# Kernel optimization log

Measured on AMD Instinct MI355X. Metric: run time of the kernel, lower is better.

Reference implementation:

```python
import jax, jax.numpy as jnp
import numpy as np
from jax import lax

NUM_LAYERS = 8
K = 3
C = 128  # residual/gate/skip channels
DIL_H = (1, 2, 4, 8, 1, 2, 4, 8)
DIL_W = (1, 2, 4, 8, 16, 32, 64, 128)
DN = ('NCHW', 'OIHW', 'NCHW')


def _conv(x, w, b, dh=1, dw=1, pad_h=0, pad_w=0):
    # causal along H: pad only on top by pad_h (equivalent to pytorch's
    # symmetric pad + out[:, :, :-pad_h] slice); symmetric along W.
    out = lax.conv_general_dilated(
        x, w, window_strides=(1, 1),
        padding=((pad_h, 0), (pad_w, pad_w)),
        rhs_dilation=(dh, dw), dimension_numbers=DN)
    return out + b[None, :, None, None]


def setup_inputs() -> dict:
    key = jax.random.key(0)
    ks = jax.random.split(key, 6)
    B, H, W = 2, 16, 4096
    return {
        'x': jax.random.normal(ks[0], (B, 1, H, W), jnp.float32),
        'c': jax.random.normal(ks[1], (B, 80, H, W), jnp.float32),
        'front_w': jax.random.normal(ks[2], (C, 1, 1, 1), jnp.float32),
        'front_b': jnp.zeros((C,), jnp.float32),
        'fg_w': jax.random.normal(ks[3], (NUM_LAYERS, 2 * C, C, K, K), jnp.float32) * (1.0 / np.sqrt(C * K * K)),
        'fg_b': jnp.zeros((NUM_LAYERS, 2 * C), jnp.float32),
        'fgc_w': jax.random.normal(ks[4], (NUM_LAYERS, 2 * C, 80, 1, 1), jnp.float32) * (1.0 / np.sqrt(80)),
        'fgc_b': jnp.zeros((NUM_LAYERS, 2 * C), jnp.float32),
        'rs_w': jax.random.normal(ks[5], (NUM_LAYERS, 2 * C, C, 1, 1), jnp.float32) * (1.0 / np.sqrt(C)),
        'rs_b': jnp.zeros((NUM_LAYERS, 2 * C), jnp.float32),
    }


def reference(x, c, front_w, front_b, fg_w, fg_b, fgc_w, fgc_b, rs_w, rs_b):
    # front 1x1 conv (causal but pad_h = 0 for kernel_size=1)
    h = _conv(x, front_w, front_b)  # [B, C, H, W]
    skip = jnp.zeros_like(h)
    for i in range(NUM_LAYERS):
        dh, dw = DIL_H[i], DIL_W[i]
        pad_h = dh * (K - 1)
        pad_w = dw * (K - 1) // 2
        # dilated causal conv -> [B, 2C, H, W]
        hg = _conv(h, fg_w[i], fg_b[i], dh, dw, pad_h, pad_w)
        # 1x1 conditioning conv on c
        cg = _conv(c, fgc_w[i], fgc_b[i])
        a = hg + cg
        acts = jnp.tanh(a[:, :C]) * jax.nn.sigmoid(a[:, C:])
        # 1x1 res/skip conv -> [B, 2C, H, W]
        rs = _conv(acts, rs_w[i], rs_b[i])
        h = h + rs[:, :C]
        skip = skip + rs[:, C:]
    return skip
```

## Files before the change

### kernel.cpp

```cpp
#include <hip/hip_runtime.h>
#include <math.h>

#define NL    8
#define CCH   128
#define CINC  80
#define CPAD  128
#define HH    16
#define WW    4096
#define HW    (HH*WW)
#define PADW  128
#define WWP   (WW + 2*PADW)
#define NT    10
#define PADF  64

#define HBF_N   (2*HH*WWP*CCH)
#define ZROW_N  (WWP*CCH)
#define CT_N    (2*HW*CPAD)
#define SKB_N   (2*HW*CCH)
#define GW_N    (NL*NT*4*16*64*8)
#define RW_N    (NL*4*16*64*8)

using v8s   = __attribute__((ext_vector_type(8))) short;
using f32x4 = __attribute__((ext_vector_type(4))) float;

__device__ __forceinline__ unsigned short f2bf(float f) {
    unsigned int u = __builtin_bit_cast(unsigned int, f);
    u += 0x7fffu + ((u >> 16) & 1u);
    return (unsigned short)(u >> 16);
}
__device__ __forceinline__ float bfu2f(unsigned int v) {
    return __builtin_bit_cast(float, v << 16);
}
__device__ __forceinline__ float gated(float a, float g) {
    float ac = fminf(a, 15.0f);
    float e  = __expf(2.0f * ac);
    float th = (e - 1.0f) * __builtin_amdgcn_rcpf(e + 1.0f);
    float sg = __builtin_amdgcn_rcpf(1.0f + __expf(-g));
    return th * sg;
}

__device__ __forceinline__ void gl_lds16(const void* g, void* l) {
    __builtin_amdgcn_global_load_lds(
        (const __attribute__((address_space(1))) unsigned int*)g,
        (__attribute__((address_space(3))) unsigned int*)l, 16, 0, 0);
}

__device__ __host__ __forceinline__ int tap_of(int t) { return (t < 7) ? t : (t == 8 ? 8 : 7); }

__global__ void prep_weights(const float* __restrict__ fg_w, const float* __restrict__ fgc_w,
                             const float* __restrict__ rs_w,
                             const float* __restrict__ fg_b, const float* __restrict__ fgc_b,
                             const float* __restrict__ rs_b,
                             unsigned short* __restrict__ gw, unsigned short* __restrict__ rw,
                             float* __restrict__ gbias, float* __restrict__ rbias) {
    const int total = GW_N + RW_N + 2 * NL * 256;
    const int stride = gridDim.x * blockDim.x;
    for (int idx = blockIdx.x * blockDim.x + threadIdx.x; idx < total; idx += stride) {
        if (idx < GW_N) {
            int t0 = idx;
            int j = t0 & 7;  t0 >>= 3;
            int l = t0 & 63; t0 >>= 6;
            int mt = t0 & 15; t0 >>= 4;
            int tq = t0 % (NT*4);
            int i  = t0 / (NT*4);
            int t  = tq >> 2, q = tq & 3;
            int m  = mt*16 + (l & 15);
            int oo = (m & 1)*128 + (m >> 1);
            int ci = q*32 + 8*(l >> 4) + j;
            float v;
            if (t == 7) {
                v = (ci < CINC) ? fgc_w[((size_t)i*256 + oo)*CINC + ci] : 0.0f;
            } else {
                int tt = tap_of(t);
                v = fg_w[(((size_t)i*256 + oo)*128 + ci)*9 + tt];
            }
            gw[idx] = f2bf(v);
        } else if (idx < GW_N + RW_N) {
            int t0 = idx - GW_N;
            int j = t0 & 7;  t0 >>= 3;
            int l = t0 & 63; t0 >>= 6;
            int mt = t0 & 15; t0 >>= 4;
            int q = t0 & 3;
            int i = t0 >> 2;
            int m  = mt*16 + (l & 15);
            int oo = (m & 1)*128 + (m >> 1);
            int ci = q*32 + 8*(l >> 4) + j;
            rw[idx - GW_N] = f2bf(rs_w[((size_t)i*256 + oo)*128 + ci]);
        } else {
            int t0 = idx - GW_N - RW_N;
            if (t0 < NL*256) {
                int i = t0 >> 8, m = t0 & 255;
                int oo = (m & 1)*128 + (m >> 1);
                gbias[t0] = fg_b[i*256 + oo] + fgc_b[i*256 + oo];
            } else {
                t0 -= NL*256;
                int i = t0 >> 8, m = t0 & 255;
                int oo = (m & 1)*128 + (m >> 1);
                rbias[t0] = rs_b[i*256 + oo];
            }
        }
    }
}

__global__ void front_kernel(const float* __restrict__ xsrc,
                             const float* __restrict__ fw, const float* __restrict__ fb,
                             unsigned short* __restrict__ hbf0,
                             unsigned short* __restrict__ hbf1, unsigned short* __restrict__ zrow) {
    const int stride = gridDim.x * blockDim.x;
    const int t0 = blockIdx.x * blockDim.x + threadIdx.x;
    for (int idx = t0; idx < HBF_N; idx += stride) {
        int c = idx & 127;
        int rest = idx >> 7;
        int xp = rest % WWP; rest /= WWP;
        int y = rest & 15;
        int b = rest >> 4;
        int x = xp - PADW;
        if (x >= 0 && x < WW)
            hbf0[idx] = f2bf(fw[c] * xsrc[((size_t)(b*HH + y))*WW + x] + fb[c]);
        else
            hbf0[idx] = 0;
    }
    const int PADN = 2*HH*2*PADW*CCH;
    for (int idx = t0; idx < PADN; idx += stride) {
        int c = idx & 127;
        int r = idx >> 7;
        int xo = r % (2*PADW); r /= (2*PADW);
        int y = r & 15;
        int b = r >> 4;
        int xp = (xo < PADW) ? xo : xo + WW;
        hbf1[(((size_t)(b*HH + y))*WWP + xp)*CCH + c] = 0;
    }
    for (int idx = t0; idx < ZROW_N; idx += stride) zrow[idx] = 0;
}

__global__ __launch_bounds__(256) void cond_transpose(const float* __restrict__ cin,
                                                      unsigned short* __restrict__ cT) {
    __shared__ unsigned short lt[CINC][72];
    const int tid = threadIdx.x, lane = tid & 63, w = tid >> 6;
    const int x0 = blockIdx.x * 64, y = blockIdx.y, b = blockIdx.z;
#pragma unroll
    for (int r = 0; r < 20; ++r) {
        int ci = w*20 + r;
        float v = cin[(((size_t)(b*CINC + ci))*HH + y)*WW + x0 + lane];
        lt[ci][lane] = f2bf(v);
    }
    __syncthreads();
    const int px = tid & 63, cg = tid >> 6;
    unsigned int pk[16];
#pragma unroll
    for (int kk = 0; kk < 16; ++kk) {
        int c0 = cg*32 + kk*2;
        unsigned int lo = (c0     < CINC) ? lt[c0][px]     : 0;
        unsigned int hi = (c0 + 1 < CINC) ? lt[c0 + 1][px] : 0;
        pk[kk] = lo | (hi << 16);
    }
    unsigned short* dst = cT + (((size_t)(b*HH + y))*WW + x0 + px)*CPAD + cg*32;
#pragma unroll
    for (int u = 0; u < 4; ++u)
        *(uint4*)(dst + u*8) = make_uint4(pk[u*4], pk[u*4+1], pk[u*4+2], pk[u*4+3]);
}

__global__ __launch_bounds__(256, 4) void layer_fused(
        const unsigned short* __restrict__ hin, unsigned short* __restrict__ hout,
        const unsigned short* __restrict__ zrow, const unsigned short* __restrict__ cT,
        const unsigned short* __restrict__ gw, const float* __restrict__ gbias,
        const unsigned short* __restrict__ rw, const float* __restrict__ rbias,
        unsigned short* __restrict__ skipbf, float* __restrict__ outp,
        int layer, int dh, int dw, int first) {
    __shared__ char sbuf[2 * 16384];

    const int tid = threadIdx.x, lane = tid & 63, w = tid >> 6;
    const int lrow = lane & 15, lk = lane >> 4;

    const int lin = blockIdx.x + 64*(blockIdx.y + 16*blockIdx.z);
    const int logical = (lin & 7)*256 + (lin >> 3);
    const int x0 = (logical & 63) * 64;
    const int y  = (logical >> 6) & 15;
    const int b  = logical >> 10;

    f32x4 acc[4][4];
#pragma unroll
    for (int mf = 0; mf < 4; ++mf)
#pragma unroll
        for (int nf = 0; nf < 4; ++nf) acc[mf][nf] = (f32x4){0.f, 0.f, 0.f, 0.f};

    const unsigned short* rowb[3];
#pragma unroll
    for (int kh = 0; kh < 3; ++kh) {
        int yin = y - (2 - kh)*dh;
        rowb[kh] = (yin >= 0) ? hin + ((size_t)(b*HH + yin))*WWP*CCH : zrow;
    }
    const char* cb = (const char*)(cT + (((size_t)(b*HH + y))*WW + x0)*CPAD);
    const unsigned short* gwl = gw + (((size_t)layer*NT*4*16) + w*4)*512 + lane*8;

    auto stage = [&](char* dst, const char* src) {
#pragma unroll
        for (int s = 0; s < 4; ++s) {
            unsigned o = (unsigned)(w*4 + s)*1024 + (unsigned)lane*16;
            unsigned g = o ^ (((o >> 8) & 7) << 4);
            gl_lds16(src + g, dst + (w*4 + s)*1024);
        }
    };
    auto stage_t = [&](int t) {
        const char* src;
        if (t == 7) src = cb;
        else {
            int tt = tap_of(t);
            int kh = tt / 3, kw = tt - kh*3;
            src = (const char*)(rowb[kh] + (size_t)(x0 + (kw - 1)*dw + PADW)*CCH);
        }
        stage(sbuf + (t & 1)*16384, src);
    };
    auto dsread = [&](const char* bb, int q, v8s (&bv)[4]) {
#pragma unroll
        for (int nf = 0; nf < 4; ++nf) {
            int px = nf*16 + lrow;
            int o = px*256 + ((q*64 + lk*16) ^ ((lrow & 7) << 4));
            bv[nf] = *(const v8s*)(bb + o);
        }
    };
    auto loadA = [&](int t, int q, v8s (&av)[4]) {
        const unsigned short* gq = gwl + (size_t)(t*4 + q)*16*512;
#pragma unroll
        for (int mf = 0; mf < 4; ++mf) av[mf] = *(const v8s*)(gq + mf*512);
    };
    auto mf16 = [&](v8s (&av)[4], v8s (&bv)[4]) {
        __builtin_amdgcn_s_setprio(1);
#pragma unroll
        for (int mf = 0; mf < 4; ++mf)
#pragma unroll
            for (int nf = 0; nf < 4; ++nf)
                acc[mf][nf] = __builtin_amdgcn_mfma_f32_16x16x32_bf16(av[mf], bv[nf], acc[mf][nf], 0, 0, 0);
        __builtin_amdgcn_s_setprio(0);
    };

    v8s aA[4], aB[4], bv[4];
    stage_t(0);
    loadA(0, 0, aA);
    loadA(0, 1, aB);
#pragma unroll
    for (int t = 0; t < NT; ++t) {
        asm volatile("s_waitcnt vmcnt(8)" ::: "memory");
        __builtin_amdgcn_sched_barrier(0);
        __builtin_amdgcn_s_barrier();
        __builtin_amdgcn_sched_barrier(0);
        if (t + 1 < NT) stage_t(t + 1);
        const char* bb = sbuf + (t & 1)*16384;
        dsread(bb, 0, bv); mf16(aA, bv); loadA(t, 2, aA);
        dsread(bb, 1, bv); mf16(aB, bv); loadA(t, 3, aB);
        dsread(bb, 2, bv); mf16(aA, bv); if (t + 1 < NT) loadA(t + 1, 0, aA);
        dsread(bb, 3, bv); mf16(aB, bv); if (t + 1 < NT) loadA(t + 1, 1, aB);
    }

    char* sact = sbuf;
    const float* gb = gbias + layer*256;
#pragma unroll
    for (int mf = 0; mf < 4; ++mf) {
        int m0 = w*64 + mf*16 + lk*4;
        int c0 = m0 >> 1;
        float bF0 = gb[m0], bG0 = gb[m0+1], bF1 = gb[m0+2], bG1 = gb[m0+3];
#pragma unroll
        for (int nf = 0; nf < 4; ++nf) {
            int px = nf*16 + lrow;
            float o0 = gated(acc[mf][nf][0] + bF0, acc[mf][nf][1] + bG0);
            float o1 = gated(acc[mf][nf][2] + bF1, acc[mf][nf][3] + bG1);
            unsigned int pk = (unsigned int)f2bf(o0) | ((unsigned int)f2bf(o1) << 16);
            int byte = px*256 + c0*2;
            byte ^= (px & 7) << 4;
            *(unsigned int*)(sact + byte) = pk;
        }
    }
#pragma unroll
    for (int mf = 0; mf < 4; ++mf)
#pragma unroll
        for (int nf = 0; nf < 4; ++nf) acc[mf][nf] = (f32x4){0.f, 0.f, 0.f, 0.f};
    __syncthreads();

    const unsigned short* rwl = rw + (((size_t)layer*4*16) + w*4)*512 + lane*8;
#pragma unroll
    for (int q = 0; q < 4; ++q) {
        v8s av[4];
#pragma unroll
        for (int mf = 0; mf < 4; ++mf) av[mf] = *(const v8s*)(rwl + (size_t)(q*16 + mf)*512);
        dsread(sact, q, bv);
        __builtin_amdgcn_s_setprio(1);
#pragma unroll
        for (int mf = 0; mf < 4; ++mf)
#pragma unroll
            for (int nf = 0; nf < 4; ++nf)
                acc[mf][nf] = __builtin_amdgcn_mfma_f32_16x16x32_bf16(av[mf], bv[nf], acc[mf][nf], 0, 0, 0);
        __builtin_amdgcn_s_setprio(0);
    }

    unsigned int hold[4][4];
    if (layer < NL - 1) {
#pragma unroll
        for (int mf = 0; mf < 4; ++mf) {
            int c0 = w*32 + mf*8 + lk*2;
#pragma unroll
            for (int nf = 0; nf < 4; ++nf) {
                int px = nf*16 + lrow;
                int o = px*256 + ((c0*2) ^ ((px & 7) << 4));
                hold[mf][nf] = *(const unsigned int*)(sbuf + 16384 + o);
            }
        }
    }
    __syncthreads();

    float* sresf = (float*)sbuf;
    const int cp = tid >> 4, xg = tid & 15;
    const int pxl = tid & 63, cg = tid >> 6;

    if (layer < NL - 1) {
#pragma unroll
        for (int mf = 0; mf < 4; ++mf) {
            int c0 = w*32 + mf*8 + lk*2;
            float bR0 = rbias[layer*256 + 2*c0];
            float bR1 = rbias[layer*256 + 2*(c0 + 1)];
#pragma unroll
            for (int nf = 0; nf < 4; ++nf) {
                int px = nf*16 + lrow;
                int sw = px ^ (((c0 >> 1) & 3) << 3);
                float h0 = bfu2f(hold[mf][nf] & 0xffffu);
                float h1 = __builtin_bit_cast(float, hold[mf][nf] & 0xffff0000u);
                sresf[(c0    )*PADF + sw] = h0 + acc[mf][nf][0] + bR0;
                sresf[(c0 + 1)*PADF + sw] = h1 + acc[mf][nf][2] + bR1;
            }
        }
        __syncthreads();
        {
            unsigned int pk3[16];
#pragma unroll
            for (int j = 0; j < 16; ++j) {
                int sw = pxl ^ ((j & 3) << 3);
                float lo = sresf[(cg*32 + 2*j    )*PADF + sw];
                float hi = sresf[(cg*32 + 2*j + 1)*PADF + sw];
                pk3[j] = (unsigned int)f2bf(lo) | ((unsigned int)f2bf(hi) << 16);
            }
            unsigned short* hrow = hout + (((size_t)(b*HH + y))*WWP + x0 + pxl + PADW)*CCH + cg*32;
#pragma unroll
            for (int u = 0; u < 4; ++u)
                *(uint4*)(hrow + u*8) = make_uint4(pk3[u*4], pk3[u*4+1], pk3[u*4+2], pk3[u*4+3]);
        }
        __syncthreads();
    }

#pragma unroll
    for (int mf = 0; mf < 4; ++mf) {
        int c0 = w*32 + mf*8 + lk*2;
#pragma unroll
        for (int nf = 0; nf < 4; ++nf) {
            int px = nf*16 + lrow;
            int sw = px ^ (((c0 >> 1) & 3) << 3);
            sresf[(c0    )*PADF + sw] = acc[mf][nf][1];
            sresf[(c0 + 1)*PADF + sw] = acc[mf][nf][3];
        }
    }
    __syncthreads();
#pragma unroll
    for (int it = 0; it < 8; ++it) {
        int cc = it*16 + cp;
        int sw = ((cp >> 1) & 3) << 3;
        float4 s = *(float4*)(sresf + cc*PADF + ((xg*4) ^ sw));
        float bb2 = rbias[layer*256 + 2*cc + 1];
        s.x += bb2; s.y += bb2; s.z += bb2; s.w += bb2;
        size_t p = (((size_t)(b*CCH + cc))*HH + y)*WW + x0 + xg*4;
        if (layer == NL - 1) {
            uint2 o = *(const uint2*)(skipbf + p);
            float4 r;
            r.x = s.x + bfu2f(o.x & 0xffffu);
            r.y = s.y + bfu2f(o.x >> 16);
            r.z = s.z + bfu2f(o.y & 0xffffu);
            r.w = s.w + bfu2f(o.y >> 16);
            *(float4*)(outp + p) = r;
        } else {
            if (!first) {
                uint2 o = *(const uint2*)(skipbf + p);
                s.x += bfu2f(o.x & 0xffffu);
                s.y += bfu2f(o.x >> 16);
                s.z += bfu2f(o.y & 0xffffu);
                s.w += bfu2f(o.y >> 16);
            }
            uint2 np;
            np.x = (unsigned int)f2bf(s.x) | ((unsigned int)f2bf(s.y) << 16);
            np.y = (unsigned int)f2bf(s.z) | ((unsigned int)f2bf(s.w) << 16);
            *(uint2*)(skipbf + p) = np;
        }
    }
}

extern "C" void kernel_launch(void* const* d_in, const int* in_sizes, int n_in,
                              void* d_out, int out_size, void* d_ws, size_t ws_size,
                              hipStream_t stream) {
    const float* x       = (const float*)d_in[0];
    const float* c       = (const float*)d_in[1];
    const float* front_w = (const float*)d_in[2];
    const float* front_b = (const float*)d_in[3];
    const float* fg_w    = (const float*)d_in[4];
    const float* fg_b    = (const float*)d_in[5];
    const float* fgc_w   = (const float*)d_in[6];
    const float* fgc_b   = (const float*)d_in[7];
    const float* rs_w    = (const float*)d_in[8];
    const float* rs_b    = (const float*)d_in[9];

    char* ws = (char*)d_ws;
    unsigned short* hbf0 = (unsigned short*)ws;     ws += (size_t)HBF_N * 2;
    unsigned short* hbf1 = (unsigned short*)ws;     ws += (size_t)HBF_N * 2;
    unsigned short* zrow = (unsigned short*)ws;     ws += (size_t)ZROW_N * 2;
    unsigned short* cT   = (unsigned short*)ws;     ws += (size_t)CT_N * 2;
    unsigned short* skbf = (unsigned short*)ws;     ws += (size_t)SKB_N * 2;
    unsigned short* gw   = (unsigned short*)ws;     ws += (size_t)GW_N * 2;
    unsigned short* rwq  = (unsigned short*)ws;     ws += (size_t)RW_N * 2;
    float* gbias  = (float*)ws;                     ws += (size_t)NL * 256 * 4;
    float* rbias  = (float*)ws;

    float* outp = (float*)d_out;

    prep_weights<<<2048, 256, 0, stream>>>(fg_w, fgc_w, rs_w, fg_b, fgc_b, rs_b,
                                           gw, rwq, gbias, rbias);
    front_kernel<<<2048, 256, 0, stream>>>(x, front_w, front_b, hbf0, hbf1, zrow);
    cond_transpose<<<dim3(64, 16, 2), 256, 0, stream>>>(c, cT);

    static const int DILH[NL] = {1, 2, 4, 8, 1, 2, 4, 8};
    static const int DILW[NL] = {1, 2, 4, 8, 16, 32, 64, 128};

    for (int i = 0; i < NL; ++i) {
        const unsigned short* hin = (i & 1) ? hbf1 : hbf0;
        unsigned short*       hout= (i & 1) ? hbf0 : hbf1;
        layer_fused<<<dim3(64, 16, 2), 256, 0, stream>>>(hin, hout, zrow, cT, gw, gbias,
                                                         rwq, rbias, skbf, outp,
                                                         i, DILH[i], DILW[i], i == 0 ? 1 : 0);
    }
}
```

Baseline: 834.2 us.

## Split layer kernel work across 8 waves with half-size per-wave M tiles

New measurement: 853.8 us. 2.4% more time.

```diff
diff --git a/kernel.cpp b/kernel.cpp
--- a/kernel.cpp
+++ b/kernel.cpp
@@ -160,7 +160,7 @@
         *(uint4*)(dst + u*8) = make_uint4(pk[u*4], pk[u*4+1], pk[u*4+2], pk[u*4+3]);
 }
 
-__global__ __launch_bounds__(256, 4) void layer_fused(
+__global__ __launch_bounds__(512, 4) void layer_fused(
         const unsigned short* __restrict__ hin, unsigned short* __restrict__ hout,
         const unsigned short* __restrict__ zrow, const unsigned short* __restrict__ cT,
         const unsigned short* __restrict__ gw, const float* __restrict__ gbias,
@@ -178,9 +178,9 @@
     const int y  = (logical >> 6) & 15;
     const int b  = logical >> 10;
 
-    f32x4 acc[4][4];
-#pragma unroll
-    for (int mf = 0; mf < 4; ++mf)
+    f32x4 acc[2][4];
+#pragma unroll
+    for (int mf = 0; mf < 2; ++mf)
 #pragma unroll
         for (int nf = 0; nf < 4; ++nf) acc[mf][nf] = (f32x4){0.f, 0.f, 0.f, 0.f};
 
@@ -191,16 +191,8 @@
         rowb[kh] = (yin >= 0) ? hin + ((size_t)(b*HH + yin))*WWP*CCH : zrow;
     }
     const char* cb = (const char*)(cT + (((size_t)(b*HH + y))*WW + x0)*CPAD);
-    const unsigned short* gwl = gw + (((size_t)layer*NT*4*16) + w*4)*512 + lane*8;
-
-    auto stage = [&](char* dst, const char* src) {
-#pragma unroll
-        for (int s = 0; s < 4; ++s) {
-            unsigned o = (unsigned)(w*4 + s)*1024 + (unsigned)lane*16;
-            unsigned g = o ^ (((o >> 8) & 7) << 4);
-            gl_lds16(src + g, dst + (w*4 + s)*1024);
-        }
-    };
+    const unsigned short* gwl = gw + (((size_t)layer*NT*4*16) + w*2)*512 + lane*8;
+
     auto stage_t = [&](int t) {
         const char* src;
         if (t == 7) src = cb;
@@ -209,7 +201,13 @@
             int kh = tt / 3, kw = tt - kh*3;
             src = (const char*)(rowb[kh] + (size_t)(x0 + (kw - 1)*dw + PADW)*CCH);
         }
-        stage(sbuf + (t & 1)*16384, src);
+        char* dst = sbuf + (t & 1)*16384;
+#pragma unroll
+        for (int s = 0; s < 2; ++s) {
+            unsigned o = (unsigned)(w*2 + s)*1024 + (unsigned)lane*16;
+            unsigned g = o ^ (((o >> 8) & 7) << 4);
+            gl_lds16(src + g, dst + (w*2 + s)*1024);
+        }
     };
     auto dsread = [&](const char* bb, int q, v8s (&bv)[4]) {
 #pragma unroll
@@ -219,25 +217,23 @@
             bv[nf] = *(const v8s*)(bb + o);
         }
     };
-    auto loadA = [&](int t, int q, v8s (&av)[4]) {
-        const unsigned short* gq = gwl + (size_t)(t*4 + q)*16*512;
-#pragma unroll
-        for (int mf = 0; mf < 4; ++mf) av[mf] = *(const v8s*)(gq + mf*512);
-    };
-    auto mf16 = [&](v8s (&av)[4], v8s (&bv)[4]) {
+    auto mf8 = [&](v8s (&av)[2], v8s (&bv)[4]) {
         __builtin_amdgcn_s_setprio(1);
 #pragma unroll
-        for (int mf = 0; mf < 4; ++mf)
+        for (int mf = 0; mf < 2; ++mf)
 #pragma unroll
             for (int nf = 0; nf < 4; ++nf)
                 acc[mf][nf] = __builtin_amdgcn_mfma_f32_16x16x32_bf16(av[mf], bv[nf], acc[mf][nf], 0, 0, 0);
         __builtin_amdgcn_s_setprio(0);
     };
 
-    v8s aA[4], aB[4], bv[4];
+    v8s av[4][2], bv[4];
     stage_t(0);
-    loadA(0, 0, aA);
-    loadA(0, 1, aB);
+#pragma unroll
+    for (int q = 0; q < 4; ++q)
+#pragma unroll
+        for (int mf = 0; mf < 2; ++mf)
+            av[q][mf] = *(const v8s*)(gwl + (size_t)(0*4 + q)*16*512 + mf*512);
 #pragma unroll
     for (int t = 0; t < NT; ++t) {
         asm volatile("s_waitcnt vmcnt(8)" ::: "memory");
@@ -246,17 +242,23 @@
         __builtin_amdgcn_sched_barrier(0);
         if (t + 1 < NT) stage_t(t + 1);
         const char* bb = sbuf + (t & 1)*16384;
-        dsread(bb, 0, bv); mf16(aA, bv); loadA(t, 2, aA);
-        dsread(bb, 1, bv); mf16(aB, bv); loadA(t, 3, aB);
-        dsread(bb, 2, bv); mf16(aA, bv); if (t + 1 < NT) loadA(t + 1, 0, aA);
-        dsread(bb, 3, bv); mf16(aB, bv); if (t + 1 < NT) loadA(t + 1, 1, aB);
+#pragma unroll
+        for (int q = 0; q < 4; ++q) {
+            dsread(bb, q, bv);
+            mf8(av[q], bv);
+            if (t + 1 < NT) {
+#pragma unroll
+                for (int mf = 0; mf < 2; ++mf)
+                    av[q][mf] = *(const v8s*)(gwl + (size_t)((t+1)*4 + q)*16*512 + mf*512);
+            }
+        }
     }
 
     char* sact = sbuf;
     const float* gb = gbias + layer*256;
 #pragma unroll
-    for (int mf = 0; mf < 4; ++mf) {
-        int m0 = w*64 + mf*16 + lk*4;
+    for (int mf = 0; mf < 2; ++mf) {
+        int m0 = w*32 + mf*16 + lk*4;
         int c0 = m0 >> 1;
         float bF0 = gb[m0], bG0 = gb[m0+1], bF1 = gb[m0+2], bG1 = gb[m0+3];
 #pragma unroll
@@ -271,32 +273,26 @@
         }
     }
 #pragma unroll
-    for (int mf = 0; mf < 4; ++mf)
+    for (int mf = 0; mf < 2; ++mf)
 #pragma unroll
         for (int nf = 0; nf < 4; ++nf) acc[mf][nf] = (f32x4){0.f, 0.f, 0.f, 0.f};
     __syncthreads();
 
-    const unsigned short* rwl = rw + (((size_t)layer*4*16) + w*4)*512 + lane*8;
+    const unsigned short* rwl = rw + (((size_t)layer*4*16) + w*2)*512 + lane*8;
 #pragma unroll
     for (int q = 0; q < 4; ++q) {
-        v8s av[4];
-#pragma unroll
-        for (int mf = 0; mf < 4; ++mf) av[mf] = *(const v8s*)(rwl + (size_t)(q*16 + mf)*512);
+        v8s a2[2];
+#pragma unroll
+        for (int mf = 0; mf < 2; ++mf) a2[mf] = *(const v8s*)(rwl + (size_t)(q*16 + mf)*512);
         dsread(sact, q, bv);
-        __builtin_amdgcn_s_setprio(1);
-#pragma unroll
-        for (int mf = 0; mf < 4; ++mf)
-#pragma unroll
-            for (int nf = 0; nf < 4; ++nf)
-                acc[mf][nf] = __builtin_amdgcn_mfma_f32_16x16x32_bf16(av[mf], bv[nf], acc[mf][nf], 0, 0, 0);
-        __builtin_amdgcn_s_setprio(0);
-    }
-
-    unsigned int hold[4][4];
+        mf8(a2, bv);
+    }
+
+    unsigned int hold[2][4];
     if (layer < NL - 1) {
 #pragma unroll
-        for (int mf = 0; mf < 4; ++mf) {
-            int c0 = w*32 + mf*8 + lk*2;
+        for (int mf = 0; mf < 2; ++mf) {
+            int c0 = w*16 + mf*8 + lk*2;
 #pragma unroll
             for (int nf = 0; nf < 4; ++nf) {
                 int px = nf*16 + lrow;
@@ -313,8 +309,8 @@
 
     if (layer < NL - 1) {
 #pragma unroll
-        for (int mf = 0; mf < 4; ++mf) {
-            int c0 = w*32 + mf*8 + lk*2;
+        for (int mf = 0; mf < 2; ++mf) {
+            int c0 = w*16 + mf*8 + lk*2;
             float bR0 = rbias[layer*256 + 2*c0];
             float bR1 = rbias[layer*256 + 2*(c0 + 1)];
 #pragma unroll
@@ -329,25 +325,26 @@
         }
         __syncthreads();
         {
-            unsigned int pk3[16];
-#pragma unroll
-            for (int j = 0; j < 16; ++j) {
-                int sw = pxl ^ ((j & 3) << 3);
-                float lo = sresf[(cg*32 + 2*j    )*PADF + sw];
-                float hi = sresf[(cg*32 + 2*j + 1)*PADF + sw];
+            unsigned int pk3[8];
+#pragma unroll
+            for (int j = 0; j < 8; ++j) {
+                int c0 = cg*16 + 2*j;
+                int sw = pxl ^ (((c0 >> 1) & 3) << 3);
+                float lo = sresf[(c0    )*PADF + sw];
+                float hi = sresf[(c0 + 1)*PADF + sw];
                 pk3[j] = (unsigned int)f2bf(lo) | ((unsigned int)f2bf(hi) << 16);
             }
-            unsigned short* hrow = hout + (((size_t)(b*HH + y))*WWP + x0 + pxl + PADW)*CCH + cg*32;
-#pragma unroll
-            for (int u = 0; u < 4; ++u)
+            unsigned short* hrow = hout + (((size_t)(b*HH + y))*WWP + x0 + pxl + PADW)*CCH + cg*16;
+#pragma unroll
+            for (int u = 0; u < 2; ++u)
                 *(uint4*)(hrow + u*8) = make_uint4(pk3[u*4], pk3[u*4+1], pk3[u*4+2], pk3[u*4+3]);
         }
         __syncthreads();
     }
 
 #pragma unroll
-    for (int mf = 0; mf < 4; ++mf) {
-        int c0 = w*32 + mf*8 + lk*2;
+    for (int mf = 0; mf < 2; ++mf) {
+        int c0 = w*16 + mf*8 + lk*2;
 #pragma unroll
         for (int nf = 0; nf < 4; ++nf) {
             int px = nf*16 + lrow;
@@ -358,8 +355,8 @@
     }
     __syncthreads();
 #pragma unroll
-    for (int it = 0; it < 8; ++it) {
-        int cc = it*16 + cp;
+    for (int it = 0; it < 4; ++it) {
+        int cc = it*32 + cp;
         int sw = ((cp >> 1) & 3) << 3;
         float4 s = *(float4*)(sresf + cc*PADF + ((xg*4) ^ sw));
         float bb2 = rbias[layer*256 + 2*cc + 1];
@@ -427,7 +424,7 @@
     for (int i = 0; i < NL; ++i) {
         const unsigned short* hin = (i & 1) ? hbf1 : hbf0;
         unsigned short*       hout= (i & 1) ? hbf0 : hbf1;
-        layer_fused<<<dim3(64, 16, 2), 256, 0, stream>>>(hin, hout, zrow, cT, gw, gbias,
+        layer_fused<<<dim3(64, 16, 2), 512, 0, stream>>>(hin, hout, zrow, cT, gw, gbias,
                                                          rwq, rbias, skbf, outp,
                                                          i, DILH[i], DILW[i], i == 0 ? 1 : 0);
     }
```
